# Kernel tuning notes

Measured on AMD Instinct MI355X. Metric: run time of the kernel, lower is better.

The kernel has to match this reference:

```python
import jax, jax.numpy as jnp
import numpy as np

NUM_EMBEDDINGS = 512
EMBEDDING_DIM = 64


def setup_inputs() -> dict:
    key = jax.random.key(0)
    k1, k2 = jax.random.split(key)
    z_e = jax.random.normal(k1, (32, EMBEDDING_DIM, 64, 64), dtype=jnp.float32)
    lim = 1.0 / NUM_EMBEDDINGS
    codebook = jax.random.uniform(k2, (NUM_EMBEDDINGS, EMBEDDING_DIM),
                                  dtype=jnp.float32, minval=-lim, maxval=lim)
    return {"z_e": z_e, "codebook": codebook}


def reference(z_e, codebook):
    B, C, H, W = z_e.shape
    # [B,C,H,W] -> [N, C] with N = B*H*W (channels-last flatten)
    z_flat = jnp.transpose(z_e, (0, 2, 3, 1)).reshape(-1, C)
    # squared L2 distance via ||a||^2 + ||b||^2 - 2 a.b (same math, no NxKxC tensor)
    d = (jnp.sum(z_flat * z_flat, axis=1, keepdims=True)          # [N,1]
         + jnp.sum(codebook * codebook, axis=1)[None, :]           # [1,K]
         - 2.0 * jnp.einsum('nc,kc->nk', z_flat, codebook))        # [N,K]
    encoding_indices = jnp.argmin(d, axis=1)                       # [N] int
    z_q = codebook[encoding_indices].reshape(B, H, W, C)
    z_q = jnp.transpose(z_q, (0, 3, 1, 2))                         # [B,C,H,W]
    return z_q, encoding_indices
```

## Files before the change

### kernel.cpp

```cpp
#include <hip/hip_runtime.h>
#include <stdint.h>


#pragma clang fp contract(off)

#define KCODES 512
#define CDIM 64
#define HW 4096
#define ZQ_ELEMS 8388608

static __device__ __forceinline__ float cnorm_row(const float* __restrict__ row) {
    float r[8];
    #pragma unroll
    for (int j = 0; j < 8; ++j) r[j] = row[j] * row[j];
    #pragma unroll
    for (int i = 8; i < 64; i += 8) {
        #pragma unroll
        for (int j = 0; j < 8; ++j) r[j] = r[j] + row[i + j] * row[i + j];
    }
    return ((r[0] + r[1]) + (r[2] + r[3])) + ((r[4] + r[5]) + (r[6] + r[7]));
}

__global__ void cnorm_kernel(const float* __restrict__ cb,
                             float* __restrict__ cnorm_out) {
    int k = (int)blockIdx.x * 256 + (int)threadIdx.x;
    if (k < KCODES) cnorm_out[k] = cnorm_row(cb + (size_t)k * CDIM);
}

__global__ __launch_bounds__(256)
void vq_kernel(
    const float* __restrict__ z_e,
    const float* __restrict__ cb,
    const float* __restrict__ cnorm_g,
    float* __restrict__ out)
{
    __shared__ float cnorm[KCODES];
    __shared__ float dcand[4 * 64];
    __shared__ int   kcand[4 * 64];

    if (cnorm_g) {
        #pragma unroll
        for (int k = (int)threadIdx.x; k < KCODES; k += 256)
            cnorm[k] = cnorm_g[k];
    } else {
        for (int k = (int)threadIdx.x; k < KCODES; k += 256)
            cnorm[k] = cnorm_row(cb + (size_t)k * CDIM);
    }

    const int lane = (int)threadIdx.x & 63;
    const int g = __builtin_amdgcn_readfirstlane((int)threadIdx.x >> 6);
    const int n0 = (int)blockIdx.x * 64;
    const int b = n0 / HW;
    const int hw0 = n0 % HW;
    const float* zp = z_e + (size_t)b * CDIM * HW + hw0 + lane;

    float zz[CDIM];
    #pragma unroll
    for (int m = 0; m < CDIM; ++m)
        zz[m] = zp[(size_t)m * HW];

    float sz;
    {
        float r[8];
        #pragma unroll
        for (int j = 0; j < 8; ++j) r[j] = zz[j] * zz[j];
        #pragma unroll
        for (int i = 8; i < 64; i += 8) {
            #pragma unroll
            for (int j = 0; j < 8; ++j) r[j] = r[j] + zz[i + j] * zz[i + j];
        }
        sz = ((r[0] + r[1]) + (r[2] + r[3])) + ((r[4] + r[5]) + (r[6] + r[7]));
    }

    __syncthreads();

    float best = 3.4e38f;
    int bk = 0;
    const int k0 = g * 128;

    for (int i = 0; i < 128; ++i) {
        const int k = k0 + i;
        const float* ck = cb + (size_t)k * CDIM;

        float v[16];
        #pragma unroll
        for (int l = 0; l < 16; ++l)
            v[l] = fmaf(zz[l], ck[l],
                     fmaf(zz[16 + l], ck[16 + l],
                       fmaf(zz[32 + l], ck[32 + l],
                         fmaf(zz[48 + l], ck[48 + l], 0.f))));

        float e[8];
        #pragma unroll
        for (int l = 0; l < 8; ++l) e[l] = v[l] + v[8 + l];
        float f[4];
        #pragma unroll
        for (int l = 0; l < 4; ++l) f[l] = e[l] + e[4 + l];
        float g0 = f[0] + f[2];
        float g1 = f[1] + f[3];
        float dot = g0 + g1;

        float A = sz + cnorm[k];
        float d = fmaf(dot, -2.f, A);

        if (d < best) { best = d; bk = k; }
    }

    dcand[g * 64 + lane] = best;
    kcand[g * 64 + lane] = bk;
    __syncthreads();

    float bd = dcand[lane];
    int bi = kcand[lane];
    #pragma unroll
    for (int gg = 1; gg < 4; ++gg) {
        float d2 = dcand[gg * 64 + lane];
        int   k2 = kcand[gg * 64 + lane];
        if (d2 < bd) { bd = d2; bi = k2; }
    }

    if (g == 0) out[ZQ_ELEMS + n0 + lane] = (float)bi;

    const float* row = cb + (size_t)bi * CDIM;
    float* op = out + (size_t)b * CDIM * HW + hw0 + lane;
    #pragma unroll
    for (int c = 0; c < 16; ++c) {
        const int ch = g * 16 + c;
        op[(size_t)ch * HW] = row[ch];
    }
}

extern "C" void kernel_launch(void* const* d_in, const int* in_sizes, int n_in,
                              void* d_out, int out_size, void* d_ws, size_t ws_size,
                              hipStream_t stream) {
    const float* z_e = (const float*)d_in[0];
    const float* cb  = (const float*)d_in[1];
    float* out = (float*)d_out;

    float* cnorm_ws = nullptr;
    if (ws_size >= KCODES * sizeof(float)) {
        cnorm_ws = (float*)d_ws;
        cnorm_kernel<<<dim3(2), dim3(256), 0, stream>>>(cb, cnorm_ws);
    }
    vq_kernel<<<dim3(2048), dim3(256), 0, stream>>>(z_e, cb, cnorm_ws, out);
}
```

Baseline: 195.8 us.

## Stage full codebook in LDS and process 128 pixels per 512-thread block

```diff
diff --git a/kernel.cpp b/kernel.cpp
--- a/kernel.cpp
+++ b/kernel.cpp
@@ -9,6 +9,9 @@
 #define HW 4096
 #define ZQ_ELEMS 8388608
 
+#define LDS_FLOATS 34432
+#define LDS_BYTES  (LDS_FLOATS * 4)
+
 static __device__ __forceinline__ float cnorm_row(const float* __restrict__ row) {
     float r[8];
     #pragma unroll
@@ -27,12 +30,139 @@
     if (k < KCODES) cnorm_out[k] = cnorm_row(cb + (size_t)k * CDIM);
 }
 
+__global__ __launch_bounds__(512)
+void vq_lds(const float* __restrict__ z_e,
+            const float* __restrict__ cb,
+            const float* __restrict__ cnorm_g,
+            float* __restrict__ out)
+{
+    extern __shared__ float smem[];
+    float* cbs   = smem;
+    float* cnorm = smem + 32768;
+    float* dcand = smem + 33280;
+    int*   kcand = (int*)(smem + 33792);
+    int*   kbest = (int*)(smem + 34304);
+
+    const int tid = (int)threadIdx.x;
+
+    {
+        const float4* src = (const float4*)cb;
+        float4* dst = (float4*)cbs;
+        #pragma unroll
+        for (int j = 0; j < 16; ++j)
+            dst[tid + 512 * j] = src[tid + 512 * j];
+    }
+    if (cnorm_g) {
+        if (tid < KCODES) cnorm[tid] = cnorm_g[tid];
+    } else {
+        if (tid < KCODES) cnorm[tid] = cnorm_row(cb + (size_t)tid * CDIM);
+    }
+
+    const int lane = tid & 63;
+    const int wid  = __builtin_amdgcn_readfirstlane(tid >> 6);
+    const int g    = wid & 3;
+    const int pgrp = wid >> 2;
+
+    const int n0 = (int)blockIdx.x * 128;
+    const int b = n0 / HW;
+    const int hw0 = n0 % HW;
+    const float* zp = z_e + (size_t)b * CDIM * HW + hw0 + pgrp * 64 + lane;
+
+    float zz[CDIM];
+    #pragma unroll
+    for (int m = 0; m < CDIM; ++m)
+        zz[m] = zp[(size_t)m * HW];
+
+    float sz;
+    {
+        float r[8];
+        #pragma unroll
+        for (int j = 0; j < 8; ++j) r[j] = zz[j] * zz[j];
+        #pragma unroll
+        for (int i = 8; i < 64; i += 8) {
+            #pragma unroll
+            for (int j = 0; j < 8; ++j) r[j] = r[j] + zz[i + j] * zz[i + j];
+        }
+        sz = ((r[0] + r[1]) + (r[2] + r[3])) + ((r[4] + r[5]) + (r[6] + r[7]));
+    }
+
+    __syncthreads();
+
+    float best = 3.4e38f;
+    int bk = 0;
+    const int k0 = g * 128;
+
+    #pragma unroll 2
+    for (int i = 0; i < 128; ++i) {
+        const int k = k0 + i;
+        const float4* ck4 = (const float4*)(cbs + (size_t)k * CDIM);
+
+        float r[CDIM];
+        #pragma unroll
+        for (int j = 0; j < 16; ++j) {
+            float4 t = ck4[j];
+            r[4 * j + 0] = t.x; r[4 * j + 1] = t.y;
+            r[4 * j + 2] = t.z; r[4 * j + 3] = t.w;
+        }
+
+        float v[16];
+        #pragma unroll
+        for (int l = 0; l < 16; ++l)
+            v[l] = fmaf(zz[l], r[l],
+                     fmaf(zz[16 + l], r[16 + l],
+                       fmaf(zz[32 + l], r[32 + l],
+                         fmaf(zz[48 + l], r[48 + l], 0.f))));
+
+        float e[8];
+        #pragma unroll
+        for (int l = 0; l < 8; ++l) e[l] = v[l] + v[8 + l];
+        float f[4];
+        #pragma unroll
+        for (int l = 0; l < 4; ++l) f[l] = e[l] + e[4 + l];
+        float g0 = f[0] + f[2];
+        float g1 = f[1] + f[3];
+        float dot = g0 + g1;
+
+        float A = sz + cnorm[k];
+        float d = fmaf(dot, -2.f, A);
+
+        if (d < best) { best = d; bk = k; }
+    }
+
+    dcand[pgrp * 256 + g * 64 + lane] = best;
+    kcand[pgrp * 256 + g * 64 + lane] = bk;
+    __syncthreads();
+
+    if (tid < 128) {
+        const int pg = tid >> 6, l = tid & 63;
+        float bd = dcand[pg * 256 + l];
+        int bi = kcand[pg * 256 + l];
+        #pragma unroll
+        for (int gg = 1; gg < 4; ++gg) {
+            float d2 = dcand[pg * 256 + gg * 64 + l];
+            int   k2 = kcand[pg * 256 + gg * 64 + l];
+            if (d2 < bd) { bd = d2; bi = k2; }
+        }
+        out[ZQ_ELEMS + n0 + tid] = (float)bi;
+        kbest[tid] = bi;
+    }
+    __syncthreads();
+
+    const int bi = kbest[pgrp * 64 + lane];
+    const float* row = cbs + (size_t)bi * CDIM;
+    float* op = out + (size_t)b * CDIM * HW + hw0 + pgrp * 64 + lane;
+    #pragma unroll
+    for (int c = 0; c < 16; ++c) {
+        const int ch = g * 16 + c;
+        op[(size_t)ch * HW] = row[ch];
+    }
+}
+
 __global__ __launch_bounds__(256)
-void vq_kernel(
-    const float* __restrict__ z_e,
-    const float* __restrict__ cb,
-    const float* __restrict__ cnorm_g,
-    float* __restrict__ out)
+void vq_sload(const float* __restrict__ z_e,
+              const float* __restrict__ cb,
+              const float* __restrict__ cnorm_g,
+              float* __restrict__ out)
 {
     __shared__ float cnorm[KCODES];
     __shared__ float dcand[4 * 64];
@@ -142,5 +272,17 @@
         cnorm_ws = (float*)d_ws;
         cnorm_kernel<<<dim3(2), dim3(256), 0, stream>>>(cb, cnorm_ws);
     }
-    vq_kernel<<<dim3(2048), dim3(256), 0, stream>>>(z_e, cb, cnorm_ws, out);
-}
+
+    static int lds_ok = -1;
+    if (lds_ok < 0) {
+        lds_ok = (hipFuncSetAttribute((const void*)vq_lds,
+                                      hipFuncAttributeMaxDynamicSharedMemorySize,
+                                      LDS_BYTES) == hipSuccess) ? 1 : 0;
+    }
+
+    if (lds_ok == 1) {
+        vq_lds<<<dim3(1024), dim3(512), LDS_BYTES, stream>>>(z_e, cb, cnorm_ws, out);
+    } else {
+        vq_sload<<<dim3(2048), dim3(256), 0, stream>>>(z_e, cb, cnorm_ws, out);
+    }
+}
```

New measurement: 244.2 us. +24.8%, slower.

## Use bf16 MFMA coarse distance search with exact fp32 rescoring of near-minimum candidates

Applied to the files above, without the earlier changes.

```diff
diff --git a/kernel.cpp b/kernel.cpp
--- a/kernel.cpp
+++ b/kernel.cpp
@@ -8,6 +8,23 @@
 #define CDIM 64
 #define HW 4096
 #define ZQ_ELEMS 8388608
+#define DELTA 0.01f
+
+typedef float f32x4 __attribute__((ext_vector_type(4)));
+typedef unsigned short us8 __attribute__((ext_vector_type(8)));
+
+static __device__ __forceinline__ unsigned short bf16_rne(float f) {
+    union { float f; unsigned u; } x; x.f = f;
+    unsigned lsb = (x.u >> 16) & 1u;
+    return (unsigned short)((x.u + 0x7FFFu + lsb) >> 16);
+}
+
+static __device__ __forceinline__ f32x4 mfma_bf16(us8 a, us8 b, f32x4 c) {
+    f32x4 d;
+    asm("v_mfma_f32_16x16x32_bf16 %0, %1, %2, %3"
+        : "=v"(d) : "v"(a), "v"(b), "v"(c));
+    return d;
+}
 
 static __device__ __forceinline__ float cnorm_row(const float* __restrict__ row) {
     float r[8];
@@ -22,30 +39,206 @@
 }
 
 __global__ void cnorm_kernel(const float* __restrict__ cb,
-                             float* __restrict__ cnorm_out) {
+                             float* __restrict__ ws) {
     int k = (int)blockIdx.x * 256 + (int)threadIdx.x;
-    if (k < KCODES) cnorm_out[k] = cnorm_row(cb + (size_t)k * CDIM);
+    if (k < KCODES) ws[k] = cnorm_row(cb + (size_t)k * CDIM);
+}
+
+__global__ void cbfrag_kernel(const float* __restrict__ cb,
+                              float* __restrict__ ws) {
+    int idx = (int)blockIdx.x * 256 + (int)threadIdx.x;
+    unsigned short* fr = (unsigned short*)(ws + KCODES);
+    int i  = idx & 7;
+    int ln = (idx >> 3) & 63;
+    int kh = (idx >> 9) & 1;
+    int t  = idx >> 10;
+    int code = t * 16 + (ln & 15);
+    int ch   = kh * 32 + ((ln >> 4) & 3) * 8 + i;
+    fr[idx] = bf16_rne(cb[(size_t)code * CDIM + ch]);
 }
 
 __global__ __launch_bounds__(256)
-void vq_kernel(
-    const float* __restrict__ z_e,
-    const float* __restrict__ cb,
-    const float* __restrict__ cnorm_g,
-    float* __restrict__ out)
+void vq_mfma(const float* __restrict__ z_e,
+             const float* __restrict__ cb,
+             const float* __restrict__ ws,
+             float* __restrict__ out)
+{
+    __shared__ float cnorm_s[KCODES];
+    __shared__ __align__(16) float zz_s[4][16][68];
+    __shared__ float sz_s[4][16];
+
+    const int tid  = (int)threadIdx.x;
+    const int lane = tid & 63;
+    const int wid  = tid >> 6;
+    const int grp  = lane >> 4;
+    const int col  = lane & 15;
+
+    cnorm_s[tid]       = ws[tid];
+    cnorm_s[tid + 256] = ws[tid + 256];
+    __syncthreads();
+
+    const us8* __restrict__ frag = (const us8*)(ws + KCODES);
+
+    float cnr[32];
+    #pragma unroll
+    for (int t = 0; t < 32; ++t) cnr[t] = cnorm_s[t * 16 + col];
+
+    for (int s = 0; s < 4; ++s) {
+        const int n0s = (int)blockIdx.x * 256 + wid * 64 + s * 16;
+        const int b   = n0s / HW;
+        const int hw0 = n0s % HW;
+        const float* zbase = z_e + (size_t)b * CDIM * HW + hw0;
+
+        float zv[16];
+        #pragma unroll
+        for (int kh = 0; kh < 2; ++kh)
+            #pragma unroll
+            for (int i = 0; i < 8; ++i)
+                zv[kh * 8 + i] = zbase[(size_t)(kh * 32 + grp * 8 + i) * HW + col];
+
+        #pragma unroll
+        for (int kh = 0; kh < 2; ++kh)
+            #pragma unroll
+            for (int ih = 0; ih < 2; ++ih) {
+                f32x4 t4 = { zv[kh*8 + ih*4 + 0], zv[kh*8 + ih*4 + 1],
+                             zv[kh*8 + ih*4 + 2], zv[kh*8 + ih*4 + 3] };
+                int c0 = kh * 32 + grp * 8 + ih * 4;
+                *(f32x4*)&zz_s[wid][col][c0] = t4;
+            }
+
+        us8 za0, za1;
+        #pragma unroll
+        for (int i = 0; i < 8; ++i) za0[i] = bf16_rne(-2.0f * zv[i]);
+        #pragma unroll
+        for (int i = 0; i < 8; ++i) za1[i] = bf16_rne(-2.0f * zv[8 + i]);
+
+        float r0, r1;
+        {
+            float a0 = zz_s[wid][col][2 * grp];
+            float b0 = zz_s[wid][col][2 * grp + 1];
+            r0 = a0 * a0; r1 = b0 * b0;
+            #pragma unroll
+            for (int ii = 1; ii < 8; ++ii) {
+                float av = zz_s[wid][col][ii * 8 + 2 * grp];
+                float bv = zz_s[wid][col][ii * 8 + 2 * grp + 1];
+                r0 = r0 + av * av; r1 = r1 + bv * bv;
+            }
+        }
+        float tj = r0 + r1;
+        float u  = tj + __shfl_xor(tj, 16);
+        float szp = u + __shfl_xor(u, 32);
+        if (grp == 0) sz_s[wid][col] = szp;
+
+        f32x4 acc[32];
+        #pragma unroll
+        for (int t = 0; t < 32; ++t) {
+            f32x4 ai = { cnr[t], cnr[t], cnr[t], cnr[t] };
+            us8 bf0 = frag[(t * 2 + 0) * 64 + lane];
+            us8 bf1 = frag[(t * 2 + 1) * 64 + lane];
+            f32x4 m0 = mfma_bf16(za0, bf0, ai);
+            acc[t] = mfma_bf16(za1, bf1, m0);
+        }
+
+        float mn[4];
+        #pragma unroll
+        for (int r = 0; r < 4; ++r) {
+            float m = acc[0][r];
+            #pragma unroll
+            for (int t = 1; t < 32; ++t) m = fminf(m, acc[t][r]);
+            m = fminf(m, __shfl_xor(m, 1));
+            m = fminf(m, __shfl_xor(m, 2));
+            m = fminf(m, __shfl_xor(m, 4));
+            m = fminf(m, __shfl_xor(m, 8));
+            mn[r] = m;
+        }
+
+        unsigned msk[4];
+        #pragma unroll
+        for (int r = 0; r < 4; ++r) {
+            float th = mn[r] + DELTA;
+            unsigned m = 0;
+            #pragma unroll
+            for (int t = 0; t < 32; ++t)
+                m |= (acc[t][r] <= th) ? (1u << t) : 0u;
+            msk[r] = m;
+        }
+
+        float bd[4]; int bk[4];
+        #pragma unroll
+        for (int r = 0; r < 4; ++r) {
+            bd[r] = 3.4e38f; bk[r] = 0x7fffffff;
+            const int p = grp * 4 + r;
+            unsigned m = msk[r];
+            if (m) {
+                const float szv = sz_s[wid][p];
+                const float* zzp = &zz_s[wid][p][0];
+                while (m) {
+                    int t = __builtin_ctz(m); m &= m - 1;
+                    int k = t * 16 + col;
+                    const float* ck = cb + (size_t)k * CDIM;
+                    float v[16];
+                    #pragma unroll
+                    for (int l2 = 0; l2 < 16; ++l2)
+                        v[l2] = fmaf(zzp[l2], ck[l2],
+                                 fmaf(zzp[16 + l2], ck[16 + l2],
+                                   fmaf(zzp[32 + l2], ck[32 + l2],
+                                     fmaf(zzp[48 + l2], ck[48 + l2], 0.f))));
+                    float e[8];
+                    #pragma unroll
+                    for (int l2 = 0; l2 < 8; ++l2) e[l2] = v[l2] + v[8 + l2];
+                    float f4[4];
+                    #pragma unroll
+                    for (int l2 = 0; l2 < 4; ++l2) f4[l2] = e[l2] + e[4 + l2];
+                    float g0 = f4[0] + f4[2];
+                    float g1 = f4[1] + f4[3];
+                    float dot = g0 + g1;
+                    float A = szv + cnorm_s[k];
+                    float d = fmaf(dot, -2.f, A);
+                    if (d < bd[r]) { bd[r] = d; bk[r] = k; }
+                }
+            }
+            #pragma unroll
+            for (int mlog = 0; mlog < 4; ++mlog) {
+                float od = __shfl_xor(bd[r], 1 << mlog);
+                int   ok = __shfl_xor(bk[r], 1 << mlog);
+                if (od < bd[r] || (od == bd[r] && ok < bk[r])) {
+                    bd[r] = od; bk[r] = ok;
+                }
+            }
+        }
+
+        int srcl = (col >> 2) << 4;
+        int b0v = __shfl(bk[0], srcl);
+        int b1v = __shfl(bk[1], srcl);
+        int b2v = __shfl(bk[2], srcl);
+        int b3v = __shfl(bk[3], srcl);
+        int rsel = col & 3;
+        int bkp = rsel == 0 ? b0v : rsel == 1 ? b1v : rsel == 2 ? b2v : b3v;
+
+        if (lane < 16) out[ZQ_ELEMS + n0s + lane] = (float)bkp;
+
+        const float* rowp = cb + (size_t)bkp * CDIM;
+        float* op = out + (size_t)b * CDIM * HW + hw0 + col;
+        #pragma unroll
+        for (int j = 0; j < 16; ++j) {
+            int c = grp + 4 * j;
+            op[(size_t)c * HW] = rowp[c];
+        }
+    }
+}
+
+__global__ __launch_bounds__(256)
+void vq_sload(const float* __restrict__ z_e,
+              const float* __restrict__ cb,
+              const float* __restrict__ cnorm_g,
+              float* __restrict__ out)
 {
     __shared__ float cnorm[KCODES];
     __shared__ float dcand[4 * 64];
     __shared__ int   kcand[4 * 64];
 
-    if (cnorm_g) {
-        #pragma unroll
-        for (int k = (int)threadIdx.x; k < KCODES; k += 256)
-            cnorm[k] = cnorm_g[k];
-    } else {
-        for (int k = (int)threadIdx.x; k < KCODES; k += 256)
-            cnorm[k] = cnorm_row(cb + (size_t)k * CDIM);
-    }
+    for (int k = (int)threadIdx.x; k < KCODES; k += 256)
+        cnorm[k] = cnorm_g ? cnorm_g[k] : cnorm_row(cb + (size_t)k * CDIM);
 
     const int lane = (int)threadIdx.x & 63;
     const int g = __builtin_amdgcn_readfirstlane((int)threadIdx.x >> 6);
@@ -56,8 +249,7 @@
 
     float zz[CDIM];
     #pragma unroll
-    for (int m = 0; m < CDIM; ++m)
-        zz[m] = zp[(size_t)m * HW];
+    for (int m = 0; m < CDIM; ++m) zz[m] = zp[(size_t)m * HW];
 
     float sz;
     {
@@ -81,7 +273,6 @@
     for (int i = 0; i < 128; ++i) {
         const int k = k0 + i;
         const float* ck = cb + (size_t)k * CDIM;
-
         float v[16];
         #pragma unroll
         for (int l = 0; l < 16; ++l)
@@ -89,20 +280,15 @@
                      fmaf(zz[16 + l], ck[16 + l],
                        fmaf(zz[32 + l], ck[32 + l],
                          fmaf(zz[48 + l], ck[48 + l], 0.f))));
-
         float e[8];
         #pragma unroll
         for (int l = 0; l < 8; ++l) e[l] = v[l] + v[8 + l];
         float f[4];
         #pragma unroll
         for (int l = 0; l < 4; ++l) f[l] = e[l] + e[4 + l];
-        float g0 = f[0] + f[2];
-        float g1 = f[1] + f[3];
-        float dot = g0 + g1;
-
+        float dot = (f[0] + f[2]) + (f[1] + f[3]);
         float A = sz + cnorm[k];
         float d = fmaf(dot, -2.f, A);
-
         if (d < best) { best = d; bk = k; }
     }
 
@@ -137,10 +323,13 @@
     const float* cb  = (const float*)d_in[1];
     float* out = (float*)d_out;
 
-    float* cnorm_ws = nullptr;
-    if (ws_size >= KCODES * sizeof(float)) {
-        cnorm_ws = (float*)d_ws;
-        cnorm_kernel<<<dim3(2), dim3(256), 0, stream>>>(cb, cnorm_ws);
-    }
-    vq_kernel<<<dim3(2048), dim3(256), 0, stream>>>(z_e, cb, cnorm_ws, out);
-}
+    const size_t ws_need = KCODES * 4 + 32768 * 2;
+    if (ws_size >= ws_need) {
+        float* ws = (float*)d_ws;
+        cnorm_kernel<<<dim3(2), dim3(256), 0, stream>>>(cb, ws);
+        cbfrag_kernel<<<dim3(128), dim3(256), 0, stream>>>(cb, ws);
+        vq_mfma<<<dim3(512), dim3(256), 0, stream>>>(z_e, cb, ws, out);
+    } else {
+        vq_sload<<<dim3(2048), dim3(256), 0, stream>>>(z_e, cb, nullptr, out);
+    }
+}
```

After: 251.7 us. 28.6% more time.
